# Kernel optimization log

Measured on AMD Instinct MI355X. Metric: run time of the kernel, lower is better.

The kernel has to match this reference:

```python
import jax, jax.numpy as jnp
import numpy as np

B, S, D_MODEL = 2, 2048, 2048
N_HEADS, N_KV_HEADS, D_HEAD = 32, 8, 64
INIT_STD = 0.02


def setup_inputs() -> dict:
    key = jax.random.key(0)
    k1, k2, k3, k4, k5 = jax.random.split(key, 5)
    return {
        "residual": jax.random.normal(k1, (B, S, D_MODEL), dtype=jnp.float32),
        "W_Q": jax.random.normal(k2, (N_HEADS, D_HEAD, D_MODEL), dtype=jnp.float32) * INIT_STD,
        "W_K": jax.random.normal(k3, (N_KV_HEADS, D_HEAD, D_MODEL), dtype=jnp.float32) * INIT_STD,
        "W_V": jax.random.normal(k4, (N_KV_HEADS, D_HEAD, D_MODEL), dtype=jnp.float32) * INIT_STD,
        "W_O": jax.random.normal(k5, (N_HEADS, D_HEAD, D_MODEL), dtype=jnp.float32) * INIT_STD,
    }


def reference(residual, W_Q, W_K, W_V, W_O):
    # QKV projections: residual [b,p,d] x W [n,h,d] -> [b,p,n,h]
    q = jnp.einsum('bpd,nhd->bpnh', residual, W_Q)
    k = jnp.einsum('bpd,nhd->bpnh', residual, W_K)
    v = jnp.einsum('bpd,nhd->bpnh', residual, W_V)

    # GQA: repeat_interleave kv heads up to n_heads
    rep = N_HEADS // N_KV_HEADS
    k = jnp.repeat(k, rep, axis=2)  # [b, p, n_heads, h]
    v = jnp.repeat(v, rep, axis=2)

    # scaled dot-product scores: [b, n, q, k]
    scores = jnp.einsum('bqnh,bknh->bnqk', q, k) / jnp.sqrt(jnp.float32(D_HEAD))

    # causal mask (seq_len == total_len, no cache)
    seq_len = residual.shape[1]
    causal = jnp.tril(jnp.ones((seq_len, seq_len), dtype=bool))
    scores = jnp.where(causal[None, None, :, :], scores, jnp.float32(-jnp.inf))

    pattern = jax.nn.softmax(scores, axis=-1)

    # weighted sum of values: [b, q, n, h]
    attn_out = jnp.einsum('bnqk,bknh->bqnh', pattern, v)

    # output projection: [b, q, d_model]
    out = jnp.einsum('bqnh,nhd->bqd', attn_out, W_O)
    return out
```

## Files before the change

kernel.cpp:

```cpp
#include <hip/hip_runtime.h>


typedef __attribute__((ext_vector_type(8))) short short8;
typedef __attribute__((ext_vector_type(4))) short short4v;
typedef __attribute__((ext_vector_type(4))) float f32x4;

__device__ __forceinline__ short f2bs(float f) {
  unsigned u = __float_as_uint(f);
  u = (u + 0x7fffu + ((u >> 16) & 1u)) >> 16;
  return (short)u;
}
__device__ __forceinline__ float bs2f(short s) {
  return __uint_as_float(((unsigned)(unsigned short)s) << 16);
}

__device__ __forceinline__ void async_ld16(const void* g, void* l) {
  __builtin_amdgcn_global_load_lds((__attribute__((address_space(1))) void*)(g),
                                   (__attribute__((address_space(3))) void*)(l),
                                   16, 0, 0);
}

#define BARRIER()                       \
  do {                                  \
    asm volatile("" ::: "memory");      \
    __builtin_amdgcn_s_barrier();       \
    asm volatile("" ::: "memory");      \
  } while (0)
#define LGKM0()                                          \
  do {                                                   \
    asm volatile("s_waitcnt lgkmcnt(0)" ::: "memory");   \
    __builtin_amdgcn_sched_barrier(0);                   \
  } while (0)
#define VMCNT(n) asm volatile("s_waitcnt vmcnt(" #n ")" ::: "memory")
#define MFMA16(a, b, c) \
  (c) = __builtin_amdgcn_mfma_f32_16x16x32_bf16((a), (b), (c), 0, 0, 0)

__device__ __forceinline__ short4v pk4bf16(float p0, float p1, float p2,
                                           float p3) {
  union {
    unsigned u[2];
    short4v s;
  } pk;
  asm("v_cvt_pk_bf16_f32 %0, %1, %2" : "=v"(pk.u[0]) : "v"(p0), "v"(p1));
  asm("v_cvt_pk_bf16_f32 %0, %1, %2" : "=v"(pk.u[1]) : "v"(p2), "v"(p3));
  return pk.s;
}

__device__ __forceinline__ int block_sniff_f32(const short* __restrict__ r,
                                               int* bad) {
  if (threadIdx.x == 0) *bad = 0;
  __syncthreads();
  int my = 0;
  for (int i = threadIdx.x; i < 512; i += blockDim.x) {
    float x = bs2f(r[i]);
    if (!(fabsf(x) < 100.0f)) my = 1;
  }
  if (my) atomicOr(bad, 1);
  __syncthreads();
  return *bad;
}

__global__ __launch_bounds__(256) void prep_kernel(
    const void* __restrict__ s0, const void* __restrict__ s1,
    const void* __restrict__ s2, const void* __restrict__ s3,
    short* __restrict__ d0, short* __restrict__ d1, short* __restrict__ d2,
    short* __restrict__ d3, const void* __restrict__ wo,
    short* __restrict__ wot) {
  __shared__ short tile[64][65];
  __shared__ int badsh;
  const int isf = block_sniff_f32((const short*)s0, &badsh);
  const int bid = blockIdx.x;
  if (bid < 7168) {
    long off = (long)bid * 256 + threadIdx.x;
    const void* src;
    short* dst;
    if (off < 1048576) {
      src = s0; dst = d0;
    } else if ((off -= 1048576) < 524288) {
      src = s1; dst = d1;
    } else if ((off -= 524288) < 131072) {
      src = s2; dst = d2;
    } else {
      off -= 131072; src = s3; dst = d3;
    }
    const long e = off * 8;
    short8 v;
    if (isf) {
      const float* f = (const float*)src + e;
      const f32x4 a = *(const f32x4*)(f);
      const f32x4 b = *(const f32x4*)(f + 4);
#pragma unroll
      for (int j = 0; j < 4; ++j) {
        v[j] = f2bs(a[j]);
        v[4 + j] = f2bs(b[j]);
      }
    } else {
      v = *(const short8*)((const short*)src + e);
    }
    *(short8*)(dst + e) = v;
  } else {
    const int tb = bid - 7168;
    const int bx = tb & 31, by = tb >> 5;
    const int tx = threadIdx.x & 63, ty = threadIdx.x >> 6;
#pragma unroll
    for (int i = 0; i < 16; ++i) {
      const int r = ty + i * 4;
      const size_t idx = (size_t)(by * 64 + r) * 2048 + bx * 64 + tx;
      tile[r][tx] =
          isf ? f2bs(((const float*)wo)[idx]) : ((const short*)wo)[idx];
    }
    __syncthreads();
#pragma unroll
    for (int i = 0; i < 16; ++i) {
      const int r = ty + i * 4;
      wot[(size_t)(bx * 64 + r) * 2048 + by * 64 + tx] = tile[tx][r];
    }
  }
}

__device__ __forceinline__ void gemm256x128(const short* __restrict__ A,
                                            int lda,
                                            const short* __restrict__ B,
                                            int ldb, void* __restrict__ C,
                                            int ldc, int rowBase, int colBase,
                                            int K, short* SM, int outF32,
                                            int outT, float cscale) {
  const int t = threadIdx.x;
  const int wave = t >> 6;
  const int lane = t & 63;
  const int quad = lane >> 4;
  const int m16 = lane & 15;
  const int wr = (wave >> 1) * 64;
  const int wc = (wave & 1) * 64;

  short* const As0 = SM;
  short* const As1 = SM + 16384;
  short* const Bs0 = SM + 32768;
  short* const Bs1 = SM + 40960;

  const int sr = t >> 3;
  const int sc8 = ((t & 7) ^ (sr & 7)) * 8;
  const short* aS = A + (size_t)(rowBase + sr) * lda + sc8;
  const short* bS = B + (size_t)(colBase + sr) * ldb + sc8;
  const int dOff = wave * 512;

#define STG_A(buf, rg, kt) \
  async_ld16(aS + (size_t)(rg) * lda + (kt) * 64, (buf) + (rg) * 64 + dOff)
#define STG_B(buf, rg, kt) \
  async_ld16(bS + (size_t)(rg) * ldb + (kt) * 64, (buf) + (rg) * 64 + dOff)
#define RD(buf, row0, kh)                          \
  (*(const short8*)((buf) + ((row0) + m16) * 64 +  \
                    ((((kh) * 4 + quad) ^ (m16 & 7)) * 8)))

  const int nT = K >> 6;
  STG_A(As0, 0, 0); STG_A(As0, 64, 0); STG_A(As0, 128, 0); STG_A(As0, 192, 0);
  STG_B(Bs0, 0, 0); STG_B(Bs0, 64, 0);
  if (nT > 1) {
    STG_A(As1, 0, 1); STG_A(As1, 64, 1); STG_A(As1, 128, 1); STG_A(As1, 192, 1);
    STG_B(Bs1, 0, 1); STG_B(Bs1, 64, 1);
  }

  f32x4 acc[4][4] = {};
  for (int tt = 0; tt < nT; ++tt) {
    short* const Ac = (tt & 1) ? As1 : As0;
    short* const Bc = (tt & 1) ? Bs1 : Bs0;

    if (tt + 1 < nT) {
      VMCNT(6);
    } else {
      VMCNT(0);
    }
    BARRIER();

    short8 a0[4], b0[4];
#pragma unroll
    for (int i = 0; i < 4; ++i) a0[i] = RD(Ac, wr + i * 16, 0);
#pragma unroll
    for (int j = 0; j < 4; ++j) b0[j] = RD(Bc, wc + j * 16, 0);
#pragma unroll
    for (int i = 0; i < 4; ++i)
#pragma unroll
      for (int j = 0; j < 4; ++j) MFMA16(a0[i], b0[j], acc[i][j]);

    short8 a1[4], b1[4];
#pragma unroll
    for (int i = 0; i < 4; ++i) a1[i] = RD(Ac, wr + i * 16, 1);
#pragma unroll
    for (int j = 0; j < 4; ++j) b1[j] = RD(Bc, wc + j * 16, 1);
    LGKM0();
    BARRIER();

    if (tt + 2 < nT) {
      STG_A(Ac, 0, tt + 2); STG_A(Ac, 64, tt + 2);
      STG_A(Ac, 128, tt + 2); STG_A(Ac, 192, tt + 2);
      STG_B(Bc, 0, tt + 2); STG_B(Bc, 64, tt + 2);
    }

#pragma unroll
    for (int i = 0; i < 4; ++i)
#pragma unroll
      for (int j = 0; j < 4; ++j) MFMA16(a1[i], b1[j], acc[i][j]);
  }

  float* const F = (float*)SM + wave * 4096;
#pragma unroll
  for (int i = 0; i < 4; ++i)
#pragma unroll
    for (int j = 0; j < 4; ++j)
#pragma unroll
      for (int r = 0; r < 4; ++r)
        F[(i * 16 + quad * 4 + r) * 64 + j * 16 + m16] =
            acc[i][j][r] * cscale;
  LGKM0();
  if (outT) {
    const int bb = rowBase >> 11;
    const int pBase = (rowBase & 2047) + wr;
#pragma unroll
    for (int p2 = 0; p2 < 16; ++p2) {
      const int hl = p2 * 4 + quad;
      short4v s;
#pragma unroll
      for (int r = 0; r < 4; ++r) s[r] = f2bs(F[(m16 * 4 + r) * 64 + hl]);
      *(short4v*)((short*)C + ((size_t)(bb * 512 + colBase + wc + hl)) * ldc +
                  pBase + m16 * 4) = s;
    }
  } else {
#pragma unroll
    for (int p = 0; p < 16; ++p) {
      const int row = p * 4 + quad;
      const f32x4 vv = *(const f32x4*)(F + row * 64 + m16 * 4);
      const size_t gi =
          (size_t)(rowBase + wr + row) * ldc + colBase + wc + m16 * 4;
      if (outF32) {
        *(f32x4*)((float*)C + gi) = vv;
      } else {
        short4v s;
#pragma unroll
        for (int r = 0; r < 4; ++r) s[r] = f2bs(vv[r]);
        *(short4v*)((short*)C + gi) = s;
      }
    }
  }
#undef STG_A
#undef STG_B
#undef RD
}

__global__ __launch_bounds__(512, 2) void qkv_gemm_kernel(
    const short* __restrict__ R, const short* __restrict__ WQ,
    const short* __restrict__ WK, const short* __restrict__ WV,
    short* __restrict__ q, short* __restrict__ k, short* __restrict__ vtb) {
  __shared__ __align__(16) short SM[65536];
  const int lid = blockIdx.x;
  const int nl = (lid & 7) * 48 + (lid >> 3);
  const int ct = nl % 24;
  const int rt = nl / 24;
  const short* Bm;
  short* Cout;
  int colBase, ldc, outT = 0;
  float cs = 1.0f;
  if (ct < 16) {
    Bm = WQ; Cout = q; colBase = ct * 128; ldc = 2048;
    cs = 0.125f * 1.44269504088896340736f;
  } else if (ct < 20) {
    Bm = WK; Cout = k; colBase = (ct - 16) * 128; ldc = 512;
  } else {
    Bm = WV; Cout = vtb; colBase = (ct - 20) * 128; ldc = 2048; outT = 1;
  }
  gemm256x128(R, 2048, Bm, 2048, Cout, ldc, rt * 256, colBase, 2048, SM, 0,
              outT, cs);
}

__global__ __launch_bounds__(512, 2) void out_gemm_kernel(
    const short* __restrict__ A, const short* __restrict__ Bt,
    void* __restrict__ C, const short* __restrict__ sniffsrc) {
  __shared__ __align__(16) short SM[65536];
  const int outF32 = block_sniff_f32(sniffsrc, (int*)SM);
  const int lid = blockIdx.x;
  const int nl = (lid & 7) * 32 + (lid >> 3);
  const int ct = nl & 15;
  const int rt = nl >> 4;
  gemm256x128(A, 2048, Bt, 2048, C, 2048, rt * 256, ct * 128, 2048, SM,
              outF32, 0, 1.0f);
}

__global__ __launch_bounds__(256, 3) void attn_kernel(
    const short* __restrict__ qbuf, const short* __restrict__ kbuf,
    const short* __restrict__ vtb, short* __restrict__ obuf) {
  __shared__ __align__(16) short Ks[2][64 * 64];
  __shared__ __align__(16) short Vs[2][64 * 64];
  __shared__ __align__(16) short Pb[4][32 * 64];

  const int b = blockIdx.x >> 3;
  const int kv = blockIdx.x & 7;
  const int qc = 63 - blockIdx.y;
  const int t = threadIdx.x;
  const int wave = t >> 6;
  const int hd = kv * 4 + wave;
  const int lane = t & 63;
  const int quad = lane >> 4;
  const int col = lane & 15;
  const int rb0 = qc * 32;

  short8 qf[2][2];
#pragma unroll
  for (int nt = 0; nt < 2; ++nt) {
    const int qr = rb0 + nt * 16 + col;
    const short* qp = qbuf + ((size_t)(b * 2048 + qr)) * 2048 + hd * 64 + quad * 8;
    qf[nt][0] = *(const short8*)(qp);
    qf[nt][1] = *(const short8*)(qp + 32);
  }

  short8 ones;
#pragma unroll
  for (int i = 0; i < 8; ++i) ones[i] = (short)0x3F80;

  f32x4 oacc[2][4] = {};
  f32x4 sacc[2] = {};

  short* P = &Pb[wave][0];
  const int swz = 4 * (col & 3);

  const int sRow = t >> 3;
  const int sPos = t & 7;
  const int r1 = sRow + 32;
  const short* kRow0 = kbuf + ((size_t)(b * 2048 + sRow)) * 512 + kv * 64 +
                       ((sPos ^ (sRow & 7)) * 8);
  const short* kRow1 = kbuf + ((size_t)(b * 2048 + r1)) * 512 + kv * 64 +
                       ((sPos ^ (r1 & 7)) * 8);
  const short* vRow0 = vtb + ((size_t)(b * 512 + kv * 64 + sRow)) * 2048 +
                       ((sPos ^ (sRow & 7)) * 8);
  const short* vRow1 = vtb + ((size_t)(b * 512 + kv * 64 + r1)) * 2048 +
                       ((sPos ^ (r1 & 7)) * 8);

  const int nkt = (qc >> 1) + 1;

  async_ld16(kRow0, &Ks[0][wave * 512]);
  async_ld16(kRow1, &Ks[0][2048 + wave * 512]);
  async_ld16(vRow0, &Vs[0][wave * 512]);
  async_ld16(vRow1, &Vs[0][2048 + wave * 512]);

  for (int kt = 0; kt < nkt; ++kt) {
    __syncthreads();
    if (kt + 1 < nkt) {
      const int nb = (kt + 1) & 1;
      const size_t ko = (size_t)(kt + 1) * 64 * 512;
      const int vo = (kt + 1) * 64;
      async_ld16(kRow0 + ko, &Ks[nb][wave * 512]);
      async_ld16(kRow1 + ko, &Ks[nb][2048 + wave * 512]);
      async_ld16(vRow0 + vo, &Vs[nb][wave * 512]);
      async_ld16(vRow1 + vo, &Vs[nb][2048 + wave * 512]);
    }
    const int ktb = kt * 64;
    const short* ks = &Ks[kt & 1][0];
    const short* vs = &Vs[kt & 1][0];

    short8 kf[4][2];
#pragma unroll
    for (int mt = 0; mt < 4; ++mt) {
      const int krow = mt * 16 + col;
      kf[mt][0] = *(const short8*)(ks + krow * 64 + ((quad ^ (col & 7)) * 8));
      kf[mt][1] = *(const short8*)(ks + krow * 64 + (((4 + quad) ^ (col & 7)) * 8));
    }

#pragma unroll
    for (int nt = 0; nt < 2; ++nt) {
      const int rb = rb0 + nt * 16;

      f32x4 st[4];
#pragma unroll
      for (int mt = 0; mt < 4; ++mt) {
        f32x4 z = {0.f, 0.f, 0.f, 0.f};
        z = __builtin_amdgcn_mfma_f32_16x16x32_bf16(kf[mt][0], qf[nt][0], z, 0, 0, 0);
        z = __builtin_amdgcn_mfma_f32_16x16x32_bf16(kf[mt][1], qf[nt][1], z, 0, 0, 0);
        st[mt] = z;
      }

      if (ktb + 63 > rb) {
        const int qrow = rb + col;
#pragma unroll
        for (int mt = 0; mt < 4; ++mt)
#pragma unroll
          for (int r = 0; r < 4; ++r)
            if (ktb + mt * 16 + quad * 4 + r > qrow) st[mt][r] = -1.0e30f;
      }

#pragma unroll
      for (int mt = 0; mt < 4; ++mt) {
        const float p0 = exp2f(st[mt][0]);
        const float p1 = exp2f(st[mt][1]);
        const float p2 = exp2f(st[mt][2]);
        const float p3 = exp2f(st[mt][3]);
        *(short4v*)(P + (nt * 16 + col) * 64 + (quad + 4 * (mt ^ (col & 3))) * 4) =
            pk4bf16(p0, p1, p2, p3);
      }
    }

    asm volatile("s_waitcnt lgkmcnt(0)" ::: "memory");

    short8 pf[2][2];
#pragma unroll
    for (int nt = 0; nt < 2; ++nt) {
      const int base = (nt * 16 + col) * 64;
      pf[nt][0] = *(const short8*)(P + base + ((2 * quad) ^ swz) * 4);
      pf[nt][1] = *(const short8*)(P + base + ((8 + 2 * quad) ^ swz) * 4);
    }

#pragma unroll
    for (int nt = 0; nt < 2; ++nt) {
      sacc[nt] = __builtin_amdgcn_mfma_f32_16x16x32_bf16(ones, pf[nt][0],
                                                         sacc[nt], 0, 0, 0);
      sacc[nt] = __builtin_amdgcn_mfma_f32_16x16x32_bf16(ones, pf[nt][1],
                                                         sacc[nt], 0, 0, 0);
    }

#pragma unroll
    for (int ct = 0; ct < 4; ++ct) {
      const int h = ct * 16 + col;
      const short8 va = *(const short8*)(vs + h * 64 + ((quad ^ (col & 7)) * 8));
      const short8 vb = *(const short8*)(vs + h * 64 + (((4 + quad) ^ (col & 7)) * 8));
#pragma unroll
      for (int nt = 0; nt < 2; ++nt) {
        oacc[nt][ct] = __builtin_amdgcn_mfma_f32_16x16x32_bf16(
            va, pf[nt][0], oacc[nt][ct], 0, 0, 0);
        oacc[nt][ct] = __builtin_amdgcn_mfma_f32_16x16x32_bf16(
            vb, pf[nt][1], oacc[nt][ct], 0, 0, 0);
      }
    }
  }

  const float inv0 = 1.0f / sacc[0][0];
  const float inv1 = 1.0f / sacc[1][0];
#pragma unroll
  for (int nt = 0; nt < 2; ++nt) {
    const float inv = nt ? inv1 : inv0;
#pragma unroll
    for (int ct = 0; ct < 4; ++ct) {
      *(short4v*)(P + (nt * 16 + col) * 64 + ct * 16 + quad * 4) =
          pk4bf16(oacc[nt][ct][0] * inv, oacc[nt][ct][1] * inv,
                  oacc[nt][ct][2] * inv, oacc[nt][ct][3] * inv);
    }
  }
  asm volatile("s_waitcnt lgkmcnt(0)" ::: "memory");
#pragma unroll
  for (int p = 0; p < 4; ++p) {
    const int qlocal = (lane >> 3) + 8 * p;
    const short8 row = *(const short8*)(P + qlocal * 64 + (lane & 7) * 8);
    *(short8*)(obuf + ((size_t)(b * 2048 + rb0 + qlocal)) * 2048 + hd * 64 +
               (lane & 7) * 8) = row;
  }
}

extern "C" void kernel_launch(void* const* d_in, const int* in_sizes, int n_in,
                              void* d_out, int out_size, void* d_ws,
                              size_t ws_size, hipStream_t stream) {
  char* ws = (char*)d_ws;
  short* rbuf = (short*)(ws + 256);
  short* wqb = rbuf + 8388608;
  short* wkb = wqb + 4194304;
  short* wvb = wkb + 1048576;
  short* kbuf = wvb + 1048576;
  short* vtb = kbuf + 2097152;
  short* abuf = vtb + 2097152;
  short* wot = abuf + 8388608;
  short* qbuf = (short*)d_out;

  hipLaunchKernelGGL(prep_kernel, dim3(8192), dim3(256), 0, stream,
                     d_in[0], d_in[1], d_in[2], d_in[3], rbuf, wqb, wkb, wvb,
                     d_in[4], wot);
  hipLaunchKernelGGL(qkv_gemm_kernel, dim3(384), dim3(512), 0, stream,
                     rbuf, wqb, wkb, wvb, qbuf, kbuf, vtb);
  hipLaunchKernelGGL(attn_kernel, dim3(16, 64), dim3(256), 0, stream,
                     qbuf, kbuf, vtb, abuf);
  hipLaunchKernelGGL(out_gemm_kernel, dim3(256), dim3(512), 0, stream,
                     abuf, wot, (void*)d_out, (const short*)d_in[0]);
}
```

Measured before the change: 289.3 us.

## Split V transpose into separate kernel and stagger K/V async loads in attention

Removes the transposed-output epilogue from the QKV GEMM so V is written row-major, then adds a small LDS-tiled transpose kernel that writes V^T into the now-free WQ workspace. In the attention loop, the next K tile is prefetched at the top of the iteration and the next V tile only after the score phase, with explicit vmcnt waits and raw barriers replacing __syncthreads. This aims to remove the uncoalesced strided stores in the GEMM epilogue and to overlap the K and V loads with compute. The cost is an extra kernel launch plus an extra round trip of V through memory, and the attention loop now has two barriers per iteration.

```diff
diff --git a/kernel.cpp b/kernel.cpp
--- a/kernel.cpp
+++ b/kernel.cpp
@@ -124,7 +124,7 @@
                                             int ldb, void* __restrict__ C,
                                             int ldc, int rowBase, int colBase,
                                             int K, short* SM, int outF32,
-                                            int outT, float cscale) {
+                                            float cscale) {
   const int t = threadIdx.x;
   const int wave = t >> 6;
   const int lane = t & 63;
@@ -212,33 +212,19 @@
         F[(i * 16 + quad * 4 + r) * 64 + j * 16 + m16] =
             acc[i][j][r] * cscale;
   LGKM0();
-  if (outT) {
-    const int bb = rowBase >> 11;
-    const int pBase = (rowBase & 2047) + wr;
-#pragma unroll
-    for (int p2 = 0; p2 < 16; ++p2) {
-      const int hl = p2 * 4 + quad;
+#pragma unroll
+  for (int p = 0; p < 16; ++p) {
+    const int row = p * 4 + quad;
+    const f32x4 vv = *(const f32x4*)(F + row * 64 + m16 * 4);
+    const size_t gi =
+        (size_t)(rowBase + wr + row) * ldc + colBase + wc + m16 * 4;
+    if (outF32) {
+      *(f32x4*)((float*)C + gi) = vv;
+    } else {
       short4v s;
 #pragma unroll
-      for (int r = 0; r < 4; ++r) s[r] = f2bs(F[(m16 * 4 + r) * 64 + hl]);
-      *(short4v*)((short*)C + ((size_t)(bb * 512 + colBase + wc + hl)) * ldc +
-                  pBase + m16 * 4) = s;
-    }
-  } else {
-#pragma unroll
-    for (int p = 0; p < 16; ++p) {
-      const int row = p * 4 + quad;
-      const f32x4 vv = *(const f32x4*)(F + row * 64 + m16 * 4);
-      const size_t gi =
-          (size_t)(rowBase + wr + row) * ldc + colBase + wc + m16 * 4;
-      if (outF32) {
-        *(f32x4*)((float*)C + gi) = vv;
-      } else {
-        short4v s;
-#pragma unroll
-        for (int r = 0; r < 4; ++r) s[r] = f2bs(vv[r]);
-        *(short4v*)((short*)C + gi) = s;
-      }
+      for (int r = 0; r < 4; ++r) s[r] = f2bs(vv[r]);
+      *(short4v*)((short*)C + gi) = s;
     }
   }
 #undef STG_A
@@ -249,7 +235,7 @@
 __global__ __launch_bounds__(512, 2) void qkv_gemm_kernel(
     const short* __restrict__ R, const short* __restrict__ WQ,
     const short* __restrict__ WK, const short* __restrict__ WV,
-    short* __restrict__ q, short* __restrict__ k, short* __restrict__ vtb) {
+    short* __restrict__ q, short* __restrict__ k, short* __restrict__ v) {
   __shared__ __align__(16) short SM[65536];
   const int lid = blockIdx.x;
   const int nl = (lid & 7) * 48 + (lid >> 3);
@@ -257,7 +243,7 @@
   const int rt = nl / 24;
   const short* Bm;
   short* Cout;
-  int colBase, ldc, outT = 0;
+  int colBase, ldc;
   float cs = 1.0f;
   if (ct < 16) {
     Bm = WQ; Cout = q; colBase = ct * 128; ldc = 2048;
@@ -265,10 +251,10 @@
   } else if (ct < 20) {
     Bm = WK; Cout = k; colBase = (ct - 16) * 128; ldc = 512;
   } else {
-    Bm = WV; Cout = vtb; colBase = (ct - 20) * 128; ldc = 2048; outT = 1;
+    Bm = WV; Cout = v; colBase = (ct - 20) * 128; ldc = 512;
   }
   gemm256x128(R, 2048, Bm, 2048, Cout, ldc, rt * 256, colBase, 2048, SM, 0,
-              outT, cs);
+              cs);
 }
 
 __global__ __launch_bounds__(512, 2) void out_gemm_kernel(
@@ -281,7 +267,25 @@
   const int ct = nl & 15;
   const int rt = nl >> 4;
   gemm256x128(A, 2048, Bt, 2048, C, 2048, rt * 256, ct * 128, 2048, SM,
-              outF32, 0, 1.0f);
+              outF32, 1.0f);
+}
+
+__global__ __launch_bounds__(256) void vt_kernel(const short* __restrict__ v,
+                                                 short* __restrict__ vt) {
+  __shared__ short tile[64][65];
+  const int hb = blockIdx.x * 64, pb = blockIdx.y * 64, b = blockIdx.z;
+  const int tx = threadIdx.x & 63, ty = threadIdx.x >> 6;
+#pragma unroll
+  for (int i = 0; i < 16; ++i) {
+    const int r = ty + i * 4;
+    tile[r][tx] = v[((size_t)(b * 2048 + pb + r)) * 512 + hb + tx];
+  }
+  __syncthreads();
+#pragma unroll
+  for (int i = 0; i < 16; ++i) {
+    const int r = ty + i * 4;
+    vt[((size_t)(b * 512 + hb + r)) * 2048 + pb + tx] = tile[tx][r];
+  }
 }
 
 __global__ __launch_bounds__(256, 3) void attn_kernel(
@@ -341,15 +345,13 @@
   async_ld16(vRow1, &Vs[0][2048 + wave * 512]);
 
   for (int kt = 0; kt < nkt; ++kt) {
-    __syncthreads();
+    const int nb = (kt + 1) & 1;
+    VMCNT(2);
+    BARRIER();
     if (kt + 1 < nkt) {
-      const int nb = (kt + 1) & 1;
       const size_t ko = (size_t)(kt + 1) * 64 * 512;
-      const int vo = (kt + 1) * 64;
       async_ld16(kRow0 + ko, &Ks[nb][wave * 512]);
       async_ld16(kRow1 + ko, &Ks[nb][2048 + wave * 512]);
-      async_ld16(vRow0 + vo, &Vs[nb][wave * 512]);
-      async_ld16(vRow1 + vo, &Vs[nb][2048 + wave * 512]);
     }
     const int ktb = kt * 64;
     const short* ks = &Ks[kt & 1][0];
@@ -396,7 +398,19 @@
       }
     }
 
-    asm volatile("s_waitcnt lgkmcnt(0)" ::: "memory");
+    LGKM0();
+
+    if (kt + 1 < nkt) {
+      VMCNT(2);
+    } else {
+      VMCNT(0);
+    }
+    BARRIER();
+    if (kt + 1 < nkt) {
+      const int vo = (kt + 1) * 64;
+      async_ld16(vRow0 + vo, &Vs[nb][wave * 512]);
+      async_ld16(vRow1 + vo, &Vs[nb][2048 + wave * 512]);
+    }
 
     short8 pf[2][2];
 #pragma unroll
@@ -460,16 +474,19 @@
   short* wkb = wqb + 4194304;
   short* wvb = wkb + 1048576;
   short* kbuf = wvb + 1048576;
-  short* vtb = kbuf + 2097152;
-  short* abuf = vtb + 2097152;
+  short* vbuf = kbuf + 2097152;
+  short* abuf = vbuf + 2097152;
   short* wot = abuf + 8388608;
+  short* vtb = wqb;
   short* qbuf = (short*)d_out;
 
   hipLaunchKernelGGL(prep_kernel, dim3(8192), dim3(256), 0, stream,
                      d_in[0], d_in[1], d_in[2], d_in[3], rbuf, wqb, wkb, wvb,
                      d_in[4], wot);
   hipLaunchKernelGGL(qkv_gemm_kernel, dim3(384), dim3(512), 0, stream,
-                     rbuf, wqb, wkb, wvb, qbuf, kbuf, vtb);
+                     rbuf, wqb, wkb, wvb, qbuf, kbuf, vbuf);
+  hipLaunchKernelGGL(vt_kernel, dim3(8, 32, 2), dim3(256), 0, stream,
+                     vbuf, vtb);
   hipLaunchKernelGGL(attn_kernel, dim3(16, 64), dim3(256), 0, stream,
                      qbuf, kbuf, vtb, abuf);
   hipLaunchKernelGGL(out_gemm_kernel, dim3(256), dim3(512), 0, stream,
```

Result: faster. 275.5 us (-4.8%).
